# Kernel optimization log

Measured on AMD Instinct MI355X. Metric: run time of the kernel, lower is better.

Reference implementation:

```python
import jax, jax.numpy as jnp
import numpy as np
import math

IN_FEATURES = 1024
OUT_FEATURES = 1024
RANK = 16
ALPHA = 16.0
SCALING = ALPHA / RANK


def setup_inputs() -> dict:
    key = jax.random.key(0)
    k_x, k_w, k_b, k_a, k_bb = jax.random.split(key, 5)
    x = jax.random.normal(k_x, (8, 4096, IN_FEATURES), dtype=jnp.float32)
    # frozen linear params (W: [out, in], b: [out])
    W = jax.random.normal(k_w, (OUT_FEATURES, IN_FEATURES), dtype=jnp.float32) / math.sqrt(IN_FEATURES)
    b = jax.random.normal(k_b, (OUT_FEATURES,), dtype=jnp.float32) * 0.01
    # kaiming-uniform-like init for A; B nonzero here so the LoRA path is exercised
    bound = 1.0 / math.sqrt(IN_FEATURES)
    lora_A = jax.random.uniform(k_a, (RANK, IN_FEATURES), minval=-bound, maxval=bound, dtype=jnp.float32)
    lora_B = jax.random.normal(k_bb, (OUT_FEATURES, RANK), dtype=jnp.float32) * 0.02
    return {"x": x, "W": W, "b": b, "lora_A": lora_A, "lora_B": lora_B}


def reference(x, W, b, lora_A, lora_B):
    # y = x @ W^T + b + scaling * ((x @ A^T) @ B^T)
    # (mathematically identical to F.linear(x, B @ A); chained form avoids the
    #  full-rank [out, in] materialization)
    base = jnp.einsum("bsi,oi->bso", x, W) + b
    xa = jnp.einsum("bsi,ri->bsr", x, lora_A)      # [B, S, rank]
    lora_out = jnp.einsum("bsr,or->bso", xa, lora_B) * SCALING
    return base + lora_out
```

## Files before the change

kernel.cpp:

```cpp
#include <hip/hip_runtime.h>
#include <hip/hip_bf16.h>


typedef __bf16 bf16;
typedef bf16 bf16x8 __attribute__((ext_vector_type(8)));
typedef float f32x4 __attribute__((ext_vector_type(4)));

constexpr int K_DIM = 1024;
constexpr int N_DIM = 1024;
constexpr int M_DIM = 8 * 4096;
constexpr int NT = K_DIM / 64;
constexpr float SCALING = 16.0f / 16.0f;

__global__ __launch_bounds__(256) void weff_kernel(
    const float* __restrict__ W, const float* __restrict__ A,
    const float* __restrict__ B, bf16* __restrict__ weff) {
  const int o = blockIdx.x;
  const int tid = threadIdx.x;
  float br[16];
#pragma unroll
  for (int r = 0; r < 16; ++r) br[r] = B[o * 16 + r];
#pragma unroll
  for (int j = 0; j < 4; ++j) {
    const int k = tid + j * 256;
    float s = W[o * K_DIM + k];
#pragma unroll
    for (int r = 0; r < 16; ++r) s += SCALING * br[r] * A[r * K_DIM + k];
    weff[o * K_DIM + k] = (bf16)s;
  }
}

__device__ __forceinline__ void async16(const void* g, void* l) {
  __builtin_amdgcn_global_load_lds(
      (const __attribute__((address_space(1))) void*)g,
      (__attribute__((address_space(3))) void*)l, 16, 0, 0);
}
#define BAR() __builtin_amdgcn_s_barrier()
#define LGKM(n)                                              \
  do {                                                       \
    asm volatile("s_waitcnt lgkmcnt(" #n ")" ::: "memory");  \
    __builtin_amdgcn_sched_barrier(0);                       \
  } while (0)
#define VMW(n) asm volatile("s_waitcnt vmcnt(" #n ")" ::: "memory")
#define MFMA(d, a, b) d = __builtin_amdgcn_mfma_f32_16x16x32_bf16(a, b, d, 0, 0, 0)


__global__ __launch_bounds__(512, 2) void gemm8f(
    const float* __restrict__ Xf, const bf16* __restrict__ Wf,
    const float* __restrict__ bias, float* __restrict__ Y) {
  __shared__ __align__(16) bf16 smem[65536];

  const int tid = threadIdx.x;
  const int lane = tid & 63;
  const int wid = tid >> 6;
  const int wm = wid >> 2;
  const int wn = wid & 3;
  const int l15 = lane & 15;
  const int lq = lane >> 4;

  const int bid = blockIdx.x;
  const int wgid = (bid & 7) * 64 + (bid >> 3);
  const int bm = wgid >> 2;
  const int bn = wgid & 3;
  const long m0 = (long)bm * 256;
  const int n0 = bn * 256;

  const int srow = tid >> 3;
  const int gch = (tid & 7) ^ (srow & 7);
  const bf16* wsrc = Wf + (long)(n0 + srow) * K_DIM + gch * 8;
  auto stageB = [&](int tt, int h) {
    bf16* dst = smem + (tt & 1) * 32768 + 16384 + h * 8192 + tid * 8;
    const bf16* s = wsrc + (long)h * 128 * K_DIM + tt * 64;
    async16(s, dst);
    async16(s + 64 * K_DIM, dst + 4096);
  };

  const int arow = tid >> 2;
  const int acp = tid & 3;
  const int ar7 = arow & 7;
  const int aslot0 = (2 * acp) ^ ar7;
  const int aslot1 = (2 * acp + 1) ^ ar7;
  const float* asrc = Xf + (m0 + arow) * K_DIM + acp * 16;

  f32x4 rA0[4], rA1[4];
  auto loadA0 = [&](int tt) {
    const float* s = asrc + tt * 64;
#pragma unroll
    for (int i = 0; i < 4; ++i) rA0[i] = *(const f32x4*)(s + i * 4);
  };
  auto loadA1 = [&](int tt) {
    const float* s = asrc + (long)128 * K_DIM + tt * 64;
#pragma unroll
    for (int i = 0; i < 4; ++i) rA1[i] = *(const f32x4*)(s + i * 4);
  };
  auto writeA0 = [&](int tt) {
    bf16* dst = smem + (tt & 1) * 32768 + arow * 64;
    bf16x8 c0, c1;
#pragma unroll
    for (int j = 0; j < 4; ++j) {
      c0[j] = (bf16)rA0[0][j];
      c0[4 + j] = (bf16)rA0[1][j];
      c1[j] = (bf16)rA0[2][j];
      c1[4 + j] = (bf16)rA0[3][j];
    }
    *(bf16x8*)(dst + aslot0 * 8) = c0;
    *(bf16x8*)(dst + aslot1 * 8) = c1;
  };
  auto writeA1 = [&](int tt) {
    bf16* dst = smem + (tt & 1) * 32768 + 8192 + arow * 64;
    bf16x8 c0, c1;
#pragma unroll
    for (int j = 0; j < 4; ++j) {
      c0[j] = (bf16)rA1[0][j];
      c0[4 + j] = (bf16)rA1[1][j];
      c1[j] = (bf16)rA1[2][j];
      c1[4 + j] = (bf16)rA1[3][j];
    }
    *(bf16x8*)(dst + aslot0 * 8) = c0;
    *(bf16x8*)(dst + aslot1 * 8) = c1;
  };

  const int key = l15 & 7;
  const int ck0 = lq ^ key;
  const int eA = (wm * 128 + l15) * 64 + ck0 * 8;
  const int eB = (wn * 64 + l15) * 64 + ck0 * 8;

  f32x4 acc[8][4] = {};

  loadA0(0); loadA1(0);
  stageB(0, 0); stageB(0, 1); stageB(1, 0); stageB(1, 1);
  writeA0(0); writeA1(0);
  loadA0(1); loadA1(1);
  VMW(12);
  asm volatile("s_waitcnt lgkmcnt(0)" ::: "memory");
  BAR();

  for (int t = 0; t < NT; ++t) {
    const bf16* Ab = smem + (t & 1) * 32768;
    const bf16* Bb = Ab + 16384;
    bf16x8 B0[4], B1[4];
    {
      bf16x8 A[4];
#pragma unroll
      for (int i = 0; i < 4; ++i) A[i] = *(const bf16x8*)(Ab + eA + i * 1024);
#pragma unroll
      for (int i = 0; i < 4; ++i) B0[i] = *(const bf16x8*)(Bb + eB + i * 1024);
      BAR();
      LGKM(0);
      __builtin_amdgcn_s_setprio(1);
#pragma unroll
      for (int m = 0; m < 4; ++m)
#pragma unroll
        for (int n = 0; n < 4; ++n) MFMA(acc[m][n], A[m], B0[n]);
      __builtin_amdgcn_s_setprio(0);
      BAR();
    }
    {
      bf16x8 A[4];
#pragma unroll
      for (int i = 0; i < 4; ++i)
        A[i] = *(const bf16x8*)(Ab + (eA ^ 32) + i * 1024);
#pragma unroll
      for (int i = 0; i < 4; ++i)
        B1[i] = *(const bf16x8*)(Bb + (eB ^ 32) + i * 1024);
      BAR();
      LGKM(0);
      __builtin_amdgcn_s_setprio(1);
#pragma unroll
      for (int m = 0; m < 4; ++m)
#pragma unroll
        for (int n = 0; n < 4; ++n) MFMA(acc[m][n], A[m], B1[n]);
      __builtin_amdgcn_s_setprio(0);
      BAR();
    }
    {
      bf16x8 A[4];
#pragma unroll
      for (int i = 0; i < 4; ++i)
        A[i] = *(const bf16x8*)(Ab + eA + 4096 + i * 1024);
      __builtin_amdgcn_sched_barrier(0);
      if (t < NT - 2) stageB(t + 2, 0);
      if (t < NT - 1) writeA0(t + 1);
      if (t < NT - 2) loadA0(t + 2);
      BAR();
      if (t < NT - 1) {
        LGKM(2);
      } else {
        LGKM(0);
      }
      __builtin_amdgcn_s_setprio(1);
#pragma unroll
      for (int m = 0; m < 4; ++m)
#pragma unroll
        for (int n = 0; n < 4; ++n) MFMA(acc[4 + m][n], A[m], B0[n]);
      __builtin_amdgcn_s_setprio(0);
      BAR();
    }
    {
      bf16x8 A[4];
#pragma unroll
      for (int i = 0; i < 4; ++i)
        A[i] = *(const bf16x8*)(Ab + (eA ^ 32) + 4096 + i * 1024);
      __builtin_amdgcn_sched_barrier(0);
      if (t < NT - 2) stageB(t + 2, 1);
      if (t < NT - 1) writeA1(t + 1);
      if (t < NT - 2) loadA1(t + 2);
      BAR();
      if (t < NT - 1) {
        LGKM(2);
      } else {
        LGKM(0);
      }
      __builtin_amdgcn_s_setprio(1);
#pragma unroll
      for (int m = 0; m < 4; ++m)
#pragma unroll
        for (int n = 0; n < 4; ++n) MFMA(acc[4 + m][n], A[m], B1[n]);
      __builtin_amdgcn_s_setprio(0);
      if (t < NT - 1) LGKM(0);
      if (t < NT - 2) {
        VMW(12);
      } else if (t == NT - 2) {
        VMW(0);
      }
      BAR();
    }
  }

  const long crow0 = m0 + wm * 128 + lq * 4;
  const int ccol0 = n0 + wn * 64 + l15;
  float bn4[4];
#pragma unroll
  for (int n = 0; n < 4; ++n) bn4[n] = bias[ccol0 + n * 16];
#pragma unroll
  for (int m = 0; m < 8; ++m)
#pragma unroll
    for (int n = 0; n < 4; ++n) {
      const int col = ccol0 + n * 16;
#pragma unroll
      for (int i = 0; i < 4; ++i)
        Y[(crow0 + m * 16 + i) * N_DIM + col] = acc[m][n][i] + bn4[n];
    }
}

extern "C" void kernel_launch(void* const* d_in, const int* in_sizes, int n_in,
                              void* d_out, int out_size, void* d_ws, size_t ws_size,
                              hipStream_t stream) {
  const float* x = (const float*)d_in[0];
  const float* W = (const float*)d_in[1];
  const float* b = (const float*)d_in[2];
  const float* lA = (const float*)d_in[3];
  const float* lB = (const float*)d_in[4];
  float* y = (float*)d_out;

  bf16* weff = (bf16*)d_ws;

  weff_kernel<<<dim3(1024), dim3(256), 0, stream>>>(W, lA, lB, weff);

  const int grid = (M_DIM / 256) * (N_DIM / 256);
  gemm8f<<<dim3(grid), dim3(512), 0, stream>>>(x, weff, b, y);
}
```

Measured before the change: 115.6 us.

## Make GEMM blocks process two M tiles with a continuous software pipeline

```diff
diff --git a/kernel.cpp b/kernel.cpp
--- a/kernel.cpp
+++ b/kernel.cpp
@@ -9,7 +9,7 @@
 constexpr int K_DIM = 1024;
 constexpr int N_DIM = 1024;
 constexpr int M_DIM = 8 * 4096;
-constexpr int NT = K_DIM / 64;
+constexpr int NT2 = 32;
 constexpr float SCALING = 16.0f / 16.0f;
 
 __global__ __launch_bounds__(256) void weff_kernel(
@@ -45,7 +45,7 @@
 #define MFMA(d, a, b) d = __builtin_amdgcn_mfma_f32_16x16x32_bf16(a, b, d, 0, 0, 0)
 
 
-__global__ __launch_bounds__(512, 2) void gemm8f(
+__global__ __launch_bounds__(512, 2) void gemm8p(
     const float* __restrict__ Xf, const bf16* __restrict__ Wf,
     const float* __restrict__ bias, float* __restrict__ Y) {
   __shared__ __align__(16) bf16 smem[65536];
@@ -59,10 +59,10 @@
   const int lq = lane >> 4;
 
   const int bid = blockIdx.x;
-  const int wgid = (bid & 7) * 64 + (bid >> 3);
-  const int bm = wgid >> 2;
+  const int wgid = (bid & 7) * 32 + (bid >> 3);
+  const int pairId = wgid >> 2;
   const int bn = wgid & 3;
-  const long m0 = (long)bm * 256;
+  const long m0 = (long)pairId * 512;
   const int n0 = bn * 256;
 
   const int srow = tid >> 3;
@@ -70,7 +70,7 @@
   const bf16* wsrc = Wf + (long)(n0 + srow) * K_DIM + gch * 8;
   auto stageB = [&](int tt, int h) {
     bf16* dst = smem + (tt & 1) * 32768 + 16384 + h * 8192 + tid * 8;
-    const bf16* s = wsrc + (long)h * 128 * K_DIM + tt * 64;
+    const bf16* s = wsrc + (long)h * 128 * K_DIM + (tt & 15) * 64;
     async16(s, dst);
     async16(s + 64 * K_DIM, dst + 4096);
   };
@@ -82,14 +82,18 @@
   const int aslot1 = (2 * acp + 1) ^ ar7;
   const float* asrc = Xf + (m0 + arow) * K_DIM + acp * 16;
 
+  auto abase = [&](int tt) {
+    return asrc + (long)(tt >> 4) * 256 * K_DIM + (tt & 15) * 64;
+  };
+
   f32x4 rA0[4], rA1[4];
   auto loadA0 = [&](int tt) {
-    const float* s = asrc + tt * 64;
+    const float* s = abase(tt);
 #pragma unroll
     for (int i = 0; i < 4; ++i) rA0[i] = *(const f32x4*)(s + i * 4);
   };
   auto loadA1 = [&](int tt) {
-    const float* s = asrc + (long)128 * K_DIM + tt * 64;
+    const float* s = abase(tt) + (long)128 * K_DIM;
 #pragma unroll
     for (int i = 0; i < 4; ++i) rA1[i] = *(const f32x4*)(s + i * 4);
   };
@@ -124,6 +128,16 @@
   const int ck0 = lq ^ key;
   const int eA = (wm * 128 + l15) * 64 + ck0 * 8;
   const int eB = (wn * 64 + l15) * 64 + ck0 * 8;
+
+  const long crow0 = m0 + wm * 128 + lq * 4;
+  const int ccol0 = n0 + wn * 64 + l15;
+
+  float bn4[4];
+#pragma unroll
+  for (int n = 0; n < 4; ++n) {
+    bn4[n] = bias[ccol0 + n * 16];
+    asm volatile("" ::"v"(bn4[n]));
+  }
 
   f32x4 acc[8][4] = {};
 
@@ -135,7 +149,23 @@
   asm volatile("s_waitcnt lgkmcnt(0)" ::: "memory");
   BAR();
 
-  for (int t = 0; t < NT; ++t) {
+  for (int t = 0; t < NT2; ++t) {
+    if (t == 16) {
+#pragma unroll
+      for (int m = 0; m < 8; ++m)
+#pragma unroll
+        for (int n = 0; n < 4; ++n) {
+          const int col = ccol0 + n * 16;
+#pragma unroll
+          for (int i = 0; i < 4; ++i)
+            Y[(crow0 + m * 16 + i) * N_DIM + col] = acc[m][n][i] + bn4[n];
+        }
+#pragma unroll
+      for (int m = 0; m < 8; ++m)
+#pragma unroll
+        for (int n = 0; n < 4; ++n) acc[m][n] = (f32x4)0.0f;
+    }
+
     const bf16* Ab = smem + (t & 1) * 32768;
     const bf16* Bb = Ab + 16384;
     bf16x8 B0[4], B1[4];
@@ -179,11 +209,11 @@
       for (int i = 0; i < 4; ++i)
         A[i] = *(const bf16x8*)(Ab + eA + 4096 + i * 1024);
       __builtin_amdgcn_sched_barrier(0);
-      if (t < NT - 2) stageB(t + 2, 0);
-      if (t < NT - 1) writeA0(t + 1);
-      if (t < NT - 2) loadA0(t + 2);
-      BAR();
-      if (t < NT - 1) {
+      if (t < NT2 - 2) stageB(t + 2, 0);
+      if (t < NT2 - 1) writeA0(t + 1);
+      if (t < NT2 - 2) loadA0(t + 2);
+      BAR();
+      if (t < NT2 - 1) {
         LGKM(2);
       } else {
         LGKM(0);
@@ -202,11 +232,11 @@
       for (int i = 0; i < 4; ++i)
         A[i] = *(const bf16x8*)(Ab + (eA ^ 32) + 4096 + i * 1024);
       __builtin_amdgcn_sched_barrier(0);
-      if (t < NT - 2) stageB(t + 2, 1);
-      if (t < NT - 1) writeA1(t + 1);
-      if (t < NT - 2) loadA1(t + 2);
-      BAR();
-      if (t < NT - 1) {
+      if (t < NT2 - 2) stageB(t + 2, 1);
+      if (t < NT2 - 1) writeA1(t + 1);
+      if (t < NT2 - 2) loadA1(t + 2);
+      BAR();
+      if (t < NT2 - 1) {
         LGKM(2);
       } else {
         LGKM(0);
@@ -217,21 +247,16 @@
 #pragma unroll
         for (int n = 0; n < 4; ++n) MFMA(acc[4 + m][n], A[m], B1[n]);
       __builtin_amdgcn_s_setprio(0);
-      if (t < NT - 1) LGKM(0);
-      if (t < NT - 2) {
+      if (t < NT2 - 1) LGKM(0);
+      if (t < NT2 - 2) {
         VMW(12);
-      } else if (t == NT - 2) {
+      } else if (t == NT2 - 2) {
         VMW(0);
       }
       BAR();
     }
   }
 
-  const long crow0 = m0 + wm * 128 + lq * 4;
-  const int ccol0 = n0 + wn * 64 + l15;
-  float bn4[4];
-#pragma unroll
-  for (int n = 0; n < 4; ++n) bn4[n] = bias[ccol0 + n * 16];
 #pragma unroll
   for (int m = 0; m < 8; ++m)
 #pragma unroll
@@ -239,7 +264,7 @@
       const int col = ccol0 + n * 16;
 #pragma unroll
       for (int i = 0; i < 4; ++i)
-        Y[(crow0 + m * 16 + i) * N_DIM + col] = acc[m][n][i] + bn4[n];
+        Y[(crow0 + 256 + m * 16 + i) * N_DIM + col] = acc[m][n][i] + bn4[n];
     }
 }
 
@@ -257,6 +282,6 @@
 
   weff_kernel<<<dim3(1024), dim3(256), 0, stream>>>(W, lA, lB, weff);
 
-  const int grid = (M_DIM / 256) * (N_DIM / 256);
-  gemm8f<<<dim3(grid), dim3(512), 0, stream>>>(x, weff, b, y);
-}
+  const int grid = (M_DIM / 512) * (N_DIM / 256);
+  gemm8p<<<dim3(grid), dim3(512), 0, stream>>>(x, weff, b, y);
+}
```

Result: slower. 168.6 us (+45.8%).

## Merge four per-iteration compute phases into two and drop sched barriers

Applied to the files above, without the earlier changes.

```diff
diff --git a/kernel.cpp b/kernel.cpp
--- a/kernel.cpp
+++ b/kernel.cpp
@@ -36,16 +36,12 @@
       (__attribute__((address_space(3))) void*)l, 16, 0, 0);
 }
 #define BAR() __builtin_amdgcn_s_barrier()
-#define LGKM(n)                                              \
-  do {                                                       \
-    asm volatile("s_waitcnt lgkmcnt(" #n ")" ::: "memory");  \
-    __builtin_amdgcn_sched_barrier(0);                       \
-  } while (0)
+#define LGKM(n) asm volatile("s_waitcnt lgkmcnt(" #n ")" ::: "memory")
 #define VMW(n) asm volatile("s_waitcnt vmcnt(" #n ")" ::: "memory")
 #define MFMA(d, a, b) d = __builtin_amdgcn_mfma_f32_16x16x32_bf16(a, b, d, 0, 0, 0)
 
 
-__global__ __launch_bounds__(512, 2) void gemm8f(
+__global__ __launch_bounds__(512, 2) void gemm2p(
     const float* __restrict__ Xf, const bf16* __restrict__ Wf,
     const float* __restrict__ bias, float* __restrict__ Y) {
   __shared__ __align__(16) bf16 smem[65536];
@@ -132,7 +128,7 @@
   writeA0(0); writeA1(0);
   loadA0(1); loadA1(1);
   VMW(12);
-  asm volatile("s_waitcnt lgkmcnt(0)" ::: "memory");
+  LGKM(0);
   BAR();
 
   for (int t = 0; t < NT; ++t) {
@@ -140,51 +136,44 @@
     const bf16* Bb = Ab + 16384;
     bf16x8 B0[4], B1[4];
     {
-      bf16x8 A[4];
-#pragma unroll
-      for (int i = 0; i < 4; ++i) A[i] = *(const bf16x8*)(Ab + eA + i * 1024);
-#pragma unroll
-      for (int i = 0; i < 4; ++i) B0[i] = *(const bf16x8*)(Bb + eB + i * 1024);
+      bf16x8 A0[4], A1[4];
+#pragma unroll
+      for (int i = 0; i < 4; ++i) {
+        A0[i] = *(const bf16x8*)(Ab + eA + i * 1024);
+        A1[i] = *(const bf16x8*)(Ab + (eA ^ 32) + i * 1024);
+      }
+#pragma unroll
+      for (int i = 0; i < 4; ++i) {
+        B0[i] = *(const bf16x8*)(Bb + eB + i * 1024);
+        B1[i] = *(const bf16x8*)(Bb + (eB ^ 32) + i * 1024);
+      }
       BAR();
       LGKM(0);
       __builtin_amdgcn_s_setprio(1);
 #pragma unroll
       for (int m = 0; m < 4; ++m)
 #pragma unroll
-        for (int n = 0; n < 4; ++n) MFMA(acc[m][n], A[m], B0[n]);
+        for (int n = 0; n < 4; ++n) MFMA(acc[m][n], A0[m], B0[n]);
+#pragma unroll
+      for (int m = 0; m < 4; ++m)
+#pragma unroll
+        for (int n = 0; n < 4; ++n) MFMA(acc[m][n], A1[m], B1[n]);
       __builtin_amdgcn_s_setprio(0);
       BAR();
     }
     {
-      bf16x8 A[4];
-#pragma unroll
-      for (int i = 0; i < 4; ++i)
-        A[i] = *(const bf16x8*)(Ab + (eA ^ 32) + i * 1024);
-#pragma unroll
-      for (int i = 0; i < 4; ++i)
-        B1[i] = *(const bf16x8*)(Bb + (eB ^ 32) + i * 1024);
-      BAR();
-      LGKM(0);
-      __builtin_amdgcn_s_setprio(1);
-#pragma unroll
-      for (int m = 0; m < 4; ++m)
-#pragma unroll
-        for (int n = 0; n < 4; ++n) MFMA(acc[m][n], A[m], B1[n]);
-      __builtin_amdgcn_s_setprio(0);
-      BAR();
-    }
-    {
-      bf16x8 A[4];
-#pragma unroll
-      for (int i = 0; i < 4; ++i)
-        A[i] = *(const bf16x8*)(Ab + eA + 4096 + i * 1024);
-      __builtin_amdgcn_sched_barrier(0);
-      if (t < NT - 2) stageB(t + 2, 0);
-      if (t < NT - 1) writeA0(t + 1);
-      if (t < NT - 2) loadA0(t + 2);
+      bf16x8 A0[4], A1[4];
+#pragma unroll
+      for (int i = 0; i < 4; ++i) {
+        A0[i] = *(const bf16x8*)(Ab + eA + 4096 + i * 1024);
+        A1[i] = *(const bf16x8*)(Ab + (eA ^ 32) + 4096 + i * 1024);
+      }
+      if (t < NT - 2) { stageB(t + 2, 0); stageB(t + 2, 1); }
+      if (t < NT - 1) { writeA0(t + 1); writeA1(t + 1); }
+      if (t < NT - 2) { loadA0(t + 2); loadA1(t + 2); }
       BAR();
       if (t < NT - 1) {
-        LGKM(2);
+        LGKM(4);
       } else {
         LGKM(0);
       }
@@ -192,30 +181,11 @@
 #pragma unroll
       for (int m = 0; m < 4; ++m)
 #pragma unroll
-        for (int n = 0; n < 4; ++n) MFMA(acc[4 + m][n], A[m], B0[n]);
-      __builtin_amdgcn_s_setprio(0);
-      BAR();
-    }
-    {
-      bf16x8 A[4];
-#pragma unroll
-      for (int i = 0; i < 4; ++i)
-        A[i] = *(const bf16x8*)(Ab + (eA ^ 32) + 4096 + i * 1024);
-      __builtin_amdgcn_sched_barrier(0);
-      if (t < NT - 2) stageB(t + 2, 1);
-      if (t < NT - 1) writeA1(t + 1);
-      if (t < NT - 2) loadA1(t + 2);
-      BAR();
-      if (t < NT - 1) {
-        LGKM(2);
-      } else {
-        LGKM(0);
-      }
-      __builtin_amdgcn_s_setprio(1);
-#pragma unroll
-      for (int m = 0; m < 4; ++m)
-#pragma unroll
-        for (int n = 0; n < 4; ++n) MFMA(acc[4 + m][n], A[m], B1[n]);
+        for (int n = 0; n < 4; ++n) MFMA(acc[4 + m][n], A0[m], B0[n]);
+#pragma unroll
+      for (int m = 0; m < 4; ++m)
+#pragma unroll
+        for (int n = 0; n < 4; ++n) MFMA(acc[4 + m][n], A1[m], B1[n]);
       __builtin_amdgcn_s_setprio(0);
       if (t < NT - 1) LGKM(0);
       if (t < NT - 2) {
@@ -258,5 +228,5 @@
   weff_kernel<<<dim3(1024), dim3(256), 0, stream>>>(W, lA, lB, weff);
 
   const int grid = (M_DIM / 256) * (N_DIM / 256);
-  gemm8f<<<dim3(grid), dim3(512), 0, stream>>>(x, weff, b, y);
-}
+  gemm2p<<<dim3(grid), dim3(512), 0, stream>>>(x, weff, b, y);
+}
```

After: 109.1 us. -5.7%, faster.
